# Performance work log

Measured on AMD Instinct MI355X. Metric: run time of the kernel, lower is better.

## Reference

```python
import jax, jax.numpy as jnp
import numpy as np

NUM_HEADS = 12


def _rope(t, cos, sin):
    # t: (B, H, M, D); cos/sin: (M, D//2) applied to interleaved pairs
    B, H, M, D = t.shape
    t2 = t.reshape(B, H, M, D // 2, 2)
    t0, t1 = t2[..., 0], t2[..., 1]
    c = cos[None, None]  # (1,1,M,D//2)
    s = sin[None, None]
    r0 = t0 * c - t1 * s
    r1 = t0 * s + t1 * c
    return jnp.stack([r0, r1], axis=-1).reshape(B, H, M, D)


def setup_inputs() -> dict:
    key = jax.random.key(0)
    ks = jax.random.split(key, 7)
    B, N, C = 16, 577, 768
    Hd = C // NUM_HEADS
    x = jax.random.normal(ks[0], (B, N, C), dtype=jnp.float32)
    # rotary angles for N-1 non-CLS tokens
    theta = jax.random.uniform(ks[1], (N - 1, Hd // 2), dtype=jnp.float32) * 6.28318
    cos = jnp.cos(theta)
    sin = jnp.sin(theta)
    w_qkv = jax.random.normal(ks[2], (C, 3 * C), dtype=jnp.float32) * 0.02
    b_qkv = jax.random.normal(ks[3], (3 * C,), dtype=jnp.float32) * 0.02
    w_proj = jax.random.normal(ks[4], (C, C), dtype=jnp.float32) * 0.02
    b_proj = jax.random.normal(ks[5], (C,), dtype=jnp.float32) * 0.02
    return {"x": x, "cos": cos, "sin": sin, "w_qkv": w_qkv, "b_qkv": b_qkv,
            "w_proj": w_proj, "b_proj": b_proj}


def reference(x, cos, sin, w_qkv, b_qkv, w_proj, b_proj):
    B, N, C = x.shape
    H = NUM_HEADS
    D = C // H
    scale = D ** -0.5
    qkv = x @ w_qkv + b_qkv                       # (B, N, 3C)
    qkv = qkv.reshape(B, N, 3, H, D).transpose(2, 0, 3, 1, 4)  # (3, B, H, N, D)
    q, k, v = qkv[0], qkv[1], qkv[2]
    # RoPE applied to all tokens except the CLS token (index 0)
    q = jnp.concatenate([q[:, :, :1], _rope(q[:, :, 1:], cos, sin)], axis=2)
    k = jnp.concatenate([k[:, :, :1], _rope(k[:, :, 1:], cos, sin)], axis=2)
    attn = jax.nn.softmax(jnp.einsum('bhnd,bhmd->bhnm', q, k) * scale, axis=-1)
    out = jnp.einsum('bhnm,bhmd->bhnd', attn, v)  # (B, H, N, D)
    out = out.transpose(0, 2, 1, 3).reshape(B, N, C)
    return out @ w_proj + b_proj
```

## Files before the change

kernel.cpp:

```cpp
#include <hip/hip_runtime.h>
#include <stdint.h>

typedef unsigned short u16;
typedef __attribute__((ext_vector_type(8))) short bf16x8;
typedef __attribute__((ext_vector_type(4))) float f32x4;

#define MFMA16(a, b, c) __builtin_amdgcn_mfma_f32_16x16x32_bf16((a), (b), (c), 0, 0, 0)

__device__ __forceinline__ float b2f(u16 u) {
    union { unsigned int i; float f; } v; v.i = ((unsigned int)u) << 16; return v.f;
}
__device__ __forceinline__ u16 f2b(float f) {
    union { float f; unsigned int i; } v; v.f = f;
    unsigned int r = v.i + 0x7fffu + ((v.i >> 16) & 1u);
    return (u16)(r >> 16);
}
__device__ __forceinline__ float exp2_fast(float x) {
    float r; __asm__("v_exp_f32 %0, %1" : "=v"(r) : "v"(x)); return r;
}

typedef __attribute__((address_space(1))) void gvoid;
typedef __attribute__((address_space(3))) void lvoid;
__device__ __forceinline__ void gld16(const void* g, void* l) {
    __builtin_amdgcn_global_load_lds((gvoid*)(void*)g, (lvoid*)l, 16, 0, 0);
}

__device__ __forceinline__ void tile_from_bid(int bid, int nTM, int nTN,
                                              int& rt, int& ct) {
    const int PW = 8;
    const int full = nTM / PW;
    const int per = PW * nTN;
    int p = bid / per;
    int pw = PW;
    int rem = bid - p * per;
    if (p >= full) { p = full; rem = bid - full * per; pw = nTM - full * PW; }
    const int c = rem / pw;
    const int r = rem - c * pw;
    rt = p * PW + r;
    ct = c;
}

__global__ __launch_bounds__(256) void f32_to_bf16(const float* __restrict__ in,
                                                   u16* __restrict__ out, int n) {
    const int i = (blockIdx.x * 256 + threadIdx.x) * 4;
    if (i + 3 < n) {
        const float4 v = *(const float4*)(in + i);
        ushort4 o;
        o.x = f2b(v.x); o.y = f2b(v.y); o.z = f2b(v.z); o.w = f2b(v.w);
        *(ushort4*)(out + i) = o;
    }
}

__global__ __launch_bounds__(256) void transpose_w(const float* __restrict__ wqkv,
                                                   const float* __restrict__ wproj,
                                                   u16* __restrict__ outQ,
                                                   u16* __restrict__ outP) {
    __shared__ float tile[32][33];
    int bx = blockIdx.x;
    const float* in; u16* out; int C;
    if (bx < 72) { in = wqkv; out = outQ; C = 2304; }
    else         { bx -= 72; in = wproj; out = outP; C = 768; }
    const int R = 768;
    const int t = threadIdx.x;
    const int r = t >> 3, c4 = (t & 7) * 4;
    const int ir = blockIdx.y * 32 + r, ic = bx * 32 + c4;
    const float4 v = *(const float4*)(in + (size_t)ir * C + ic);
    tile[r][c4 + 0] = v.x; tile[r][c4 + 1] = v.y;
    tile[r][c4 + 2] = v.z; tile[r][c4 + 3] = v.w;
    __syncthreads();
    const int orow = bx * 32 + r, ocol = blockIdx.y * 32 + c4;
    ushort4 o;
    o.x = f2b(tile[c4 + 0][r]); o.y = f2b(tile[c4 + 1][r]);
    o.z = f2b(tile[c4 + 2][r]); o.w = f2b(tile[c4 + 3][r]);
    *(ushort4*)(out + (size_t)orow * R + ocol) = o;
}

template <int EPI>
__global__ __launch_bounds__(512) void gemm_bt(const u16* __restrict__ A,
                                               const u16* __restrict__ Bt,
                                               const float* __restrict__ bias,
                                               void* __restrict__ Cv,
                                               const float* __restrict__ cosp,
                                               const float* __restrict__ sinp,
                                               u16* __restrict__ VtG,
                                               int M, int N, int K) {
    __shared__ __align__(16) u16 As0[128 * 64];
    __shared__ __align__(16) u16 As1[128 * 64];
    __shared__ __align__(16) u16 Bs0[128 * 64];
    __shared__ __align__(16) u16 Bs1[128 * 64];

    const int t = threadIdx.x;
    const int lane = t & 63;
    const int wave = t >> 6;
    const int l15 = lane & 15, quad = lane >> 4;
    const int wm = wave >> 2;
    const int wn = wave & 3;

    int rt, ct;
    tile_from_bid(blockIdx.y * gridDim.x + blockIdx.x, gridDim.x, gridDim.y, rt, ct);
    const int row0 = rt * 128;
    const int col0 = ct * 128;

    const f32x4 fz = {0.f, 0.f, 0.f, 0.f};
    f32x4 acc[4][2];
#pragma unroll
    for (int i = 0; i < 4; ++i)
#pragma unroll
        for (int j = 0; j < 2; ++j) acc[i][j] = fz;

    const u16* Ap[2];
    const u16* Bp[2];
    int off[2];
#pragma unroll
    for (int n = 0; n < 2; ++n) {
        const int g = t + n * 512;
        const int row = g >> 3;
        const int slot = (g & 7) ^ (row & 7);
        int ar = row0 + row; if (ar > M - 1) ar = M - 1;
        Ap[n] = A + (size_t)ar * K + slot * 8;
        Bp[n] = Bt + (size_t)(col0 + row) * K + slot * 8;
        off[n] = g * 8;
    }

#define STAGE(kt_, Ad, Bd) do {                                            \
        const int kb_ = (kt_) << 6;                                        \
        gld16(Ap[0] + kb_, (Ad) + off[0]);                                 \
        gld16(Ap[1] + kb_, (Ad) + off[1]);                                 \
        gld16(Bp[0] + kb_, (Bd) + off[0]);                                 \
        gld16(Bp[1] + kb_, (Bd) + off[1]);                                 \
    } while (0)

#define COMPUTE(Asb, Bsb) do {                                             \
        _Pragma("unroll")                                                  \
        for (int kk = 0; kk < 2; ++kk) {                                   \
            const int swk = ((kk * 4 + quad) ^ (l15 & 7)) * 8;             \
            bf16x8 af[4], bfr[2];                                          \
            _Pragma("unroll")                                              \
            for (int mi = 0; mi < 4; ++mi)                                 \
                af[mi] = *(const bf16x8*)((Asb) +                          \
                    ((wm * 4 + mi) * 16 + l15) * 64 + swk);                \
            _Pragma("unroll")                                              \
            for (int ni = 0; ni < 2; ++ni)                                 \
                bfr[ni] = *(const bf16x8*)((Bsb) +                         \
                    ((wn * 2 + ni) * 16 + l15) * 64 + swk);                \
            _Pragma("unroll")                                              \
            for (int mi = 0; mi < 4; ++mi)                                 \
                _Pragma("unroll")                                          \
                for (int ni = 0; ni < 2; ++ni)                             \
                    acc[mi][ni] = MFMA16(bfr[ni], af[mi], acc[mi][ni]);    \
        }                                                                  \
    } while (0)

    const int nKT = K >> 6;
    STAGE(0, As0, Bs0);
    __syncthreads();

    for (int kt = 0; kt < nKT; kt += 2) {
        if (kt + 1 < nKT) STAGE(kt + 1, As1, Bs1);
        COMPUTE(As0, Bs0);
        __syncthreads();
        if (kt + 2 < nKT) STAGE(kt + 2, As0, Bs0);
        COMPUTE(As1, Bs1);
        __syncthreads();
    }
#undef STAGE
#undef COMPUTE

    if (EPI == 2) {
        if (col0 >= 1536) {
#pragma unroll
            for (int mi = 0; mi < 4; ++mi) {
                const int row = row0 + wm * 64 + mi * 16 + l15;
                if (row < M) {
                    const int bb = row / 577, n = row - bb * 577;
                    u16* vdst = VtG + (size_t)bb * 491520 + n;
#pragma unroll
                    for (int ni = 0; ni < 2; ++ni) {
                        const int colb = col0 + wn * 32 + ni * 16 + quad * 4;
                        const float4 bv = *(const float4*)(bias + colb);
#pragma unroll
                        for (int r = 0; r < 4; ++r) {
                            const int cv = colb + r - 1536;
                            vdst[(size_t)(cv >> 6) * 40960 + (cv & 63) * 640] =
                                f2b(acc[mi][ni][r] + ((const float*)&bv)[r]);
                        }
                    }
                }
            }
        } else {
#pragma unroll
            for (int mi = 0; mi < 4; ++mi) {
                const int row = row0 + wm * 64 + mi * 16 + l15;
                if (row < M) {
                    const int bb = row / 577, n = row - bb * 577;
                    const bool hr = (n >= 1);
                    const float* cb = cosp + (size_t)(hr ? (n - 1) : 0) * 32;
                    const float* sb = sinp + (size_t)(hr ? (n - 1) : 0) * 32;
                    u16* outp = (u16*)Cv + (size_t)row * 1536;
#pragma unroll
                    for (int ni = 0; ni < 2; ++ni) {
                        const int colb = col0 + wn * 32 + ni * 16 + quad * 4;
                        const float4 bv = *(const float4*)(bias + colb);
                        const int pi = (colb & 63) >> 1;
                        float2 c = *(const float2*)(cb + pi);
                        float2 s = *(const float2*)(sb + pi);
                        if (!hr) { c.x = 1.f; c.y = 1.f; s.x = 0.f; s.y = 0.f; }
                        const float v0 = acc[mi][ni][0] + bv.x;
                        const float v1 = acc[mi][ni][1] + bv.y;
                        const float v2 = acc[mi][ni][2] + bv.z;
                        const float v3 = acc[mi][ni][3] + bv.w;
                        ushort4 o;
                        o.x = f2b(v0 * c.x - v1 * s.x);
                        o.y = f2b(v0 * s.x + v1 * c.x);
                        o.z = f2b(v2 * c.y - v3 * s.y);
                        o.w = f2b(v2 * s.y + v3 * c.y);
                        *(ushort4*)(outp + colb) = o;
                    }
                }
            }
        }
    } else {
#pragma unroll
        for (int ni = 0; ni < 2; ++ni) {
            const int colb = col0 + wn * 32 + ni * 16 + quad * 4;
            const float4 bv = *(const float4*)(bias + colb);
#pragma unroll
            for (int mi = 0; mi < 4; ++mi) {
                const int row = row0 + wm * 64 + mi * 16 + l15;
                if (row < M) {
                    float4 o;
                    o.x = acc[mi][ni][0] + bv.x; o.y = acc[mi][ni][1] + bv.y;
                    o.z = acc[mi][ni][2] + bv.z; o.w = acc[mi][ni][3] + bv.w;
                    *(float4*)((float*)Cv + (size_t)row * N + colb) = o;
                }
            }
        }
    }
}

#define PSTR 72
#define CEXP 0.18033688011112042f

__global__ __launch_bounds__(512, 8) void attn2(const u16* __restrict__ qkv,
                                                const u16* __restrict__ VtG,
                                                u16* __restrict__ aout) {
    __shared__ __align__(16) u16 Ks[64 * 64];
    __shared__ __align__(16) u16 Vs[64 * 64];
    __shared__ __align__(16) u16 Pb[8 * 16 * PSTR];

    const int t = threadIdx.x;
    const int lane = t & 63, wave = t >> 6;
    const int l15 = lane & 15, quad = lane >> 4;

    const int bid = blockIdx.x;
    const int swz = (bid & 7) * 120 + (bid >> 3);
    const int bh = swz / 5, qt = swz - bh * 5;
    const int b = bh / 12, h = bh - b * 12;
    const u16* baseQ = qkv + (size_t)b * 577 * 1536 + h * 64;
    const u16* baseK = baseQ + 768;
    const u16* vbase = VtG + (size_t)bh * 64 * 640;

    const int mq = qt * 128 + wave * 16 + l15;
    const int nq = mq < 577 ? mq : 576;
    bf16x8 aq[2];
    aq[0] = *(const bf16x8*)(baseQ + (size_t)nq * 1536 + quad * 8);
    aq[1] = *(const bf16x8*)(baseQ + (size_t)nq * 1536 + 32 + quad * 8);

    const int r0 = t >> 3;
    const int s0 = (t & 7) ^ (r0 & 7);
    const int o0 = t * 8;
    const u16* Kp = baseK + (size_t)r0 * 1536 + s0 * 8;
    const u16* Vp = vbase + (size_t)r0 * 640 + s0 * 8;

    const int swk0 = (quad ^ (l15 & 7)) * 8;
    const int swk1 = ((4 + quad) ^ (l15 & 7)) * 8;

    u16* Pw = Pb + wave * 16 * PSTR;

    f32x4 oacc[4];
    const f32x4 fz = {0.f, 0.f, 0.f, 0.f};
#pragma unroll
    for (int i = 0; i < 4; ++i) oacc[i] = fz;
    float m1 = -1e30f;
    float l1 = 0.f;

#define ATT_TILE(kt_, MASKED) do {                                          \
        f32x4 sacc[4];                                                      \
        _Pragma("unroll")                                                   \
        for (int nt = 0; nt < 4; ++nt) {                                    \
            sacc[nt] = fz;                                                  \
            const bf16x8 bk0 = *(const bf16x8*)(Ks + (nt * 16 + l15) * 64 + swk0); \
            sacc[nt] = MFMA16(bk0, aq[0], sacc[nt]);                        \
            const bf16x8 bk1 = *(const bf16x8*)(Ks + (nt * 16 + l15) * 64 + swk1); \
            sacc[nt] = MFMA16(bk1, aq[1], sacc[nt]);                        \
        }                                                                   \
        if (MASKED) {                                                       \
            _Pragma("unroll")                                               \
            for (int nt = 0; nt < 4; ++nt)                                  \
                _Pragma("unroll")                                           \
                for (int r = 0; r < 4; ++r)                                 \
                    if (nt * 16 + quad * 4 + r > 0) sacc[nt][r] = -1e30f;   \
        }                                                                   \
        float mA = fmaxf(fmaxf(sacc[0][0], sacc[0][1]), fmaxf(sacc[0][2], sacc[0][3])); \
        float mB = fmaxf(fmaxf(sacc[1][0], sacc[1][1]), fmaxf(sacc[1][2], sacc[1][3])); \
        float mC = fmaxf(fmaxf(sacc[2][0], sacc[2][1]), fmaxf(sacc[2][2], sacc[2][3])); \
        float mD = fmaxf(fmaxf(sacc[3][0], sacc[3][1]), fmaxf(sacc[3][2], sacc[3][3])); \
        float mt = fmaxf(fmaxf(mA, mB), fmaxf(mC, mD));                     \
        mt = fmaxf(mt, __shfl_xor(mt, 16));                                 \
        mt = fmaxf(mt, __shfl_xor(mt, 32));                                 \
        const float mnew = fmaxf(m1, mt);                                   \
        const float alpha = exp2_fast((m1 - mnew) * CEXP);                  \
        m1 = mnew;                                                          \
        const float nmc = -mnew * CEXP;                                     \
        float lsum = 0.f;                                                   \
        _Pragma("unroll")                                                   \
        for (int nt = 0; nt < 4; ++nt) {                                    \
            const float p0 = exp2_fast(__builtin_fmaf(sacc[nt][0], CEXP, nmc)); \
            const float p1 = exp2_fast(__builtin_fmaf(sacc[nt][1], CEXP, nmc)); \
            const float p2 = exp2_fast(__builtin_fmaf(sacc[nt][2], CEXP, nmc)); \
            const float p3 = exp2_fast(__builtin_fmaf(sacc[nt][3], CEXP, nmc)); \
            lsum += (p0 + p1) + (p2 + p3);                                  \
            ushort4 pk;                                                     \
            pk.x = f2b(p0); pk.y = f2b(p1); pk.z = f2b(p2); pk.w = f2b(p3); \
            *(ushort4*)(Pw + l15 * PSTR + nt * 16 + quad * 4) = pk;         \
        }                                                                   \
        _Pragma("unroll")                                                   \
        for (int dt = 0; dt < 4; ++dt) {                                    \
            oacc[dt][0] *= alpha; oacc[dt][1] *= alpha;                     \
            oacc[dt][2] *= alpha; oacc[dt][3] *= alpha;                     \
        }                                                                   \
        __asm__ __volatile__("s_waitcnt lgkmcnt(0)" ::: "memory");          \
        _Pragma("unroll")                                                   \
        for (int kc = 0; kc < 2; ++kc) {                                    \
            const bf16x8 pf = *(const bf16x8*)(Pw + l15 * PSTR + kc * 32 + quad * 8); \
            const int swkv = kc ? swk1 : swk0;                              \
            _Pragma("unroll")                                               \
            for (int dt = 0; dt < 4; ++dt) {                                \
                const bf16x8 vf = *(const bf16x8*)(Vs + (dt * 16 + l15) * 64 + swkv); \
                oacc[dt] = MFMA16(vf, pf, oacc[dt]);                        \
            }                                                               \
        }                                                                   \
        lsum += __shfl_xor(lsum, 16);                                       \
        lsum += __shfl_xor(lsum, 32);                                       \
        l1 = l1 * alpha + lsum;                                             \
    } while (0)

    for (int kt = 0; kt < 9; ++kt) {
        gld16(Kp + (size_t)kt * 98304, Ks + o0);
        gld16(Vp + kt * 64, Vs + o0);
        __syncthreads();
        ATT_TILE(kt, false);
        __syncthreads();
    }
    gld16(baseK + (size_t)576 * 1536 + s0 * 8, Ks + o0);
    gld16(Vp + 576, Vs + o0);
    __syncthreads();
    ATT_TILE(9, true);

#undef ATT_TILE

    const int n = qt * 128 + wave * 16 + l15;
    if (n < 577) {
        const float linv = 1.f / l1;
        u16* op = aout + ((size_t)b * 577 + n) * 768 + h * 64 + quad * 4;
#pragma unroll
        for (int dt = 0; dt < 4; ++dt) {
            ushort4 o;
            o.x = f2b(oacc[dt][0] * linv); o.y = f2b(oacc[dt][1] * linv);
            o.z = f2b(oacc[dt][2] * linv); o.w = f2b(oacc[dt][3] * linv);
            *(ushort4*)(op + dt * 16) = o;
        }
    }
}

extern "C" void kernel_launch(void* const* d_in, const int* in_sizes, int n_in,
                              void* d_out, int out_size, void* d_ws, size_t ws_size,
                              hipStream_t stream) {
    const float* x      = (const float*)d_in[0];
    const float* cosp   = (const float*)d_in[1];
    const float* sinp   = (const float*)d_in[2];
    const float* w_qkv  = (const float*)d_in[3];
    const float* b_qkv  = (const float*)d_in[4];
    const float* w_proj = (const float*)d_in[5];
    const float* b_proj = (const float*)d_in[6];
    float* out = (float*)d_out;

    char* ws = (char*)d_ws;
    u16* xb     = (u16*)(ws);
    u16* aout   = (u16*)(ws);
    u16* wqkvT  = (u16*)(ws + 14180352);
    u16* wprojT = (u16*)(ws + 17719296);
    u16* qkv    = (u16*)(ws + 18898944);
    u16* VtG    = (u16*)(ws + 47259648);

    f32_to_bf16<<<6924, 256, 0, stream>>>(x, xb, 7090176);
    transpose_w<<<dim3(96, 24), 256, 0, stream>>>(w_qkv, w_proj, wqkvT, wprojT);
    gemm_bt<2><<<dim3(73, 18), 512, 0, stream>>>(xb, wqkvT, b_qkv, qkv,
                                                 cosp, sinp, VtG, 9232, 2304, 768);
    attn2<<<dim3(960), 512, 0, stream>>>(qkv, VtG, aout);
    gemm_bt<1><<<dim3(73, 6), 512, 0, stream>>>(aout, wprojT, b_proj, out,
                                                nullptr, nullptr, nullptr, 9232, 768, 768);
}
```

Before: 207.1 us.

## Merge prep kernels and single-buffer GEMM LDS for higher occupancy

Fuses the x bf16 conversion and the weight transposes into one launch, so one kernel launch goes away. The GEMM drops its LDS double buffering: it now stages one K-tile, syncs, computes, and syncs again. This halves shared memory and adds a launch-bounds occupancy hint, so more workgroups fit per CU. In exchange each block loses the overlap between global loads and MFMA compute and must rely on other resident blocks to hide that latency.

```diff
diff --git a/kernel.cpp b/kernel.cpp
--- a/kernel.cpp
+++ b/kernel.cpp
@@ -40,35 +40,39 @@
     ct = c;
 }
 
-__global__ __launch_bounds__(256) void f32_to_bf16(const float* __restrict__ in,
-                                                   u16* __restrict__ out, int n) {
-    const int i = (blockIdx.x * 256 + threadIdx.x) * 4;
-    if (i + 3 < n) {
-        const float4 v = *(const float4*)(in + i);
-        ushort4 o;
-        o.x = f2b(v.x); o.y = f2b(v.y); o.z = f2b(v.z); o.w = f2b(v.w);
-        *(ushort4*)(out + i) = o;
-    }
-}
-
-__global__ __launch_bounds__(256) void transpose_w(const float* __restrict__ wqkv,
-                                                   const float* __restrict__ wproj,
-                                                   u16* __restrict__ outQ,
-                                                   u16* __restrict__ outP) {
+__global__ __launch_bounds__(256) void prep(const float* __restrict__ x,
+                                            u16* __restrict__ xb,
+                                            const float* __restrict__ wqkv,
+                                            const float* __restrict__ wproj,
+                                            u16* __restrict__ outQ,
+                                            u16* __restrict__ outP) {
     __shared__ float tile[32][33];
-    int bx = blockIdx.x;
+    const int t = threadIdx.x;
+    int bid = blockIdx.x;
+    if (bid < 6924) {
+        const int i = (bid * 256 + t) * 4;
+        if (i + 3 < 7090176) {
+            const float4 v = *(const float4*)(x + i);
+            ushort4 o;
+            o.x = f2b(v.x); o.y = f2b(v.y); o.z = f2b(v.z); o.w = f2b(v.w);
+            *(ushort4*)(xb + i) = o;
+        }
+        return;
+    }
+    bid -= 6924;
+    int bx = bid % 96;
+    const int by = bid / 96;
     const float* in; u16* out; int C;
     if (bx < 72) { in = wqkv; out = outQ; C = 2304; }
     else         { bx -= 72; in = wproj; out = outP; C = 768; }
     const int R = 768;
-    const int t = threadIdx.x;
     const int r = t >> 3, c4 = (t & 7) * 4;
-    const int ir = blockIdx.y * 32 + r, ic = bx * 32 + c4;
+    const int ir = by * 32 + r, ic = bx * 32 + c4;
     const float4 v = *(const float4*)(in + (size_t)ir * C + ic);
     tile[r][c4 + 0] = v.x; tile[r][c4 + 1] = v.y;
     tile[r][c4 + 2] = v.z; tile[r][c4 + 3] = v.w;
     __syncthreads();
-    const int orow = bx * 32 + r, ocol = blockIdx.y * 32 + c4;
+    const int orow = bx * 32 + r, ocol = by * 32 + c4;
     ushort4 o;
     o.x = f2b(tile[c4 + 0][r]); o.y = f2b(tile[c4 + 1][r]);
     o.z = f2b(tile[c4 + 2][r]); o.w = f2b(tile[c4 + 3][r]);
@@ -76,18 +80,16 @@
 }
 
 template <int EPI>
-__global__ __launch_bounds__(512) void gemm_bt(const u16* __restrict__ A,
-                                               const u16* __restrict__ Bt,
-                                               const float* __restrict__ bias,
-                                               void* __restrict__ Cv,
-                                               const float* __restrict__ cosp,
-                                               const float* __restrict__ sinp,
-                                               u16* __restrict__ VtG,
-                                               int M, int N, int K) {
-    __shared__ __align__(16) u16 As0[128 * 64];
-    __shared__ __align__(16) u16 As1[128 * 64];
-    __shared__ __align__(16) u16 Bs0[128 * 64];
-    __shared__ __align__(16) u16 Bs1[128 * 64];
+__global__ __launch_bounds__(512, 8) void gemm_bt(const u16* __restrict__ A,
+                                                  const u16* __restrict__ Bt,
+                                                  const float* __restrict__ bias,
+                                                  void* __restrict__ Cv,
+                                                  const float* __restrict__ cosp,
+                                                  const float* __restrict__ sinp,
+                                                  u16* __restrict__ VtG,
+                                                  int M, int N, int K) {
+    __shared__ __align__(16) u16 As[128 * 64];
+    __shared__ __align__(16) u16 Bs[128 * 64];
 
     const int t = threadIdx.x;
     const int lane = t & 63;
@@ -122,26 +124,26 @@
         off[n] = g * 8;
     }
 
-#define STAGE(kt_, Ad, Bd) do {                                            \
+#define STAGE(kt_) do {                                                    \
         const int kb_ = (kt_) << 6;                                        \
-        gld16(Ap[0] + kb_, (Ad) + off[0]);                                 \
-        gld16(Ap[1] + kb_, (Ad) + off[1]);                                 \
-        gld16(Bp[0] + kb_, (Bd) + off[0]);                                 \
-        gld16(Bp[1] + kb_, (Bd) + off[1]);                                 \
+        gld16(Ap[0] + kb_, As + off[0]);                                   \
+        gld16(Ap[1] + kb_, As + off[1]);                                   \
+        gld16(Bp[0] + kb_, Bs + off[0]);                                   \
+        gld16(Bp[1] + kb_, Bs + off[1]);                                   \
     } while (0)
 
-#define COMPUTE(Asb, Bsb) do {                                             \
+#define COMPUTE() do {                                                     \
         _Pragma("unroll")                                                  \
         for (int kk = 0; kk < 2; ++kk) {                                   \
             const int swk = ((kk * 4 + quad) ^ (l15 & 7)) * 8;             \
             bf16x8 af[4], bfr[2];                                          \
             _Pragma("unroll")                                              \
             for (int mi = 0; mi < 4; ++mi)                                 \
-                af[mi] = *(const bf16x8*)((Asb) +                          \
+                af[mi] = *(const bf16x8*)(As +                             \
                     ((wm * 4 + mi) * 16 + l15) * 64 + swk);                \
             _Pragma("unroll")                                              \
             for (int ni = 0; ni < 2; ++ni)                                 \
-                bfr[ni] = *(const bf16x8*)((Bsb) +                         \
+                bfr[ni] = *(const bf16x8*)(Bs +                            \
                     ((wn * 2 + ni) * 16 + l15) * 64 + swk);                \
             _Pragma("unroll")                                              \
             for (int mi = 0; mi < 4; ++mi)                                 \
@@ -152,15 +154,10 @@
     } while (0)
 
     const int nKT = K >> 6;
-    STAGE(0, As0, Bs0);
-    __syncthreads();
-
-    for (int kt = 0; kt < nKT; kt += 2) {
-        if (kt + 1 < nKT) STAGE(kt + 1, As1, Bs1);
-        COMPUTE(As0, Bs0);
+    for (int kt = 0; kt < nKT; ++kt) {
+        STAGE(kt);
         __syncthreads();
-        if (kt + 2 < nKT) STAGE(kt + 2, As0, Bs0);
-        COMPUTE(As1, Bs1);
+        COMPUTE();
         __syncthreads();
     }
 #undef STAGE
@@ -393,8 +390,7 @@
     u16* qkv    = (u16*)(ws + 18898944);
     u16* VtG    = (u16*)(ws + 47259648);
 
-    f32_to_bf16<<<6924, 256, 0, stream>>>(x, xb, 7090176);
-    transpose_w<<<dim3(96, 24), 256, 0, stream>>>(w_qkv, w_proj, wqkvT, wprojT);
+    prep<<<9228, 256, 0, stream>>>(x, xb, w_qkv, w_proj, wqkvT, wprojT);
     gemm_bt<2><<<dim3(73, 18), 512, 0, stream>>>(xb, wqkvT, b_qkv, qkv,
                                                  cosp, sinp, VtG, 9232, 2304, 768);
     attn2<<<dim3(960), 512, 0, stream>>>(qkv, VtG, aout);
```

New measurement: 221.2 us. +6.8%, slower.
